# Kernel tuning notes

Measured on AMD Instinct MI355X. Metric: run time of the kernel, lower is better.

## Reference

```python
import jax, jax.numpy as jnp
import numpy as np

CS = 5           # context_size
PAD = CS // 2    # spatial padding
EPS = 1e-12      # torch F.normalize eps


def setup_inputs() -> dict:
    key = jax.random.key(0)
    k1, k2, k3 = jax.random.split(key, 3)
    B, C, H, W = 8, 1024, 64, 64
    OC, INC = 1024, C + CS * CS  # 1049 input channels to 1x1 conv
    feature = jax.random.normal(k1, (B, C, H, W), dtype=jnp.float32)
    conv_w = jax.random.normal(k2, (OC, INC), dtype=jnp.float32) * 0.02
    conv_b = jax.random.normal(k3, (OC,), dtype=jnp.float32) * 0.02
    return {"feature": feature, "conv_w": conv_w, "conv_b": conv_b}


def reference(feature, conv_w, conv_b):
    b, c, h, w = feature.shape
    # L2-normalize over channel dim (torch normalize: x / max(||x||, eps))
    norm = jnp.sqrt(jnp.sum(feature * feature, axis=1, keepdims=True))
    fn = feature / jnp.maximum(norm, EPS)
    fp = jnp.pad(fn, ((0, 0), (0, 0), (PAD, PAD), (PAD, PAD)))
    # Windowed cosine-similarity cost volume: 25 fixed shifts (small static loop)
    sims = []
    for cc in range(CS):      # column shift (outer, matches torch ordering)
        for r in range(CS):   # row shift
            sims.append(jnp.sum(fp[:, :, r:h + r, cc:w + cc] * fn, axis=1))
    vol = jnp.stack(sims, axis=1)              # [b, 25, h, w]
    x = jnp.concatenate([feature, vol], axis=1)  # [b, c+25, h, w]
    # 1x1 conv == per-pixel GEMM over channels
    out = jnp.einsum('bihw,oi->bohw', x, conv_w) + conv_b[None, :, None, None]
    return jax.nn.relu(out)
```

## Files before the change

kernel.cpp:

```cpp
#include <hip/hip_runtime.h>
#include <stdint.h>

#define C_DIM 1024
#define HW    4096
#define KPAD  1056
#define KIN   1049
#define NPIX  32768
#define NCHUNK 16

typedef __bf16 bf16x8 __attribute__((ext_vector_type(8)));
typedef float  f32x4  __attribute__((ext_vector_type(4)));
typedef float  f32x2  __attribute__((ext_vector_type(2)));
typedef unsigned short u16x8 __attribute__((ext_vector_type(8)));

typedef const __attribute__((address_space(1))) void* gas_t;
typedef __attribute__((address_space(3))) void* las_t;

__device__ __forceinline__ unsigned short f2bf(float f) {
  unsigned u = __float_as_uint(f);
  unsigned r = u + 0x7FFFu + ((u >> 16) & 1u);
  return (unsigned short)(r >> 16);
}

__global__ __launch_bounds__(256) void prep_w(const float* __restrict__ cw,
                                              unsigned short* __restrict__ wb) {
  int o = blockIdx.x;
  for (int k = threadIdx.x; k < KPAD; k += 256) {
    float v = (k < KIN) ? cw[(size_t)o * KIN + k] : 0.0f;
    wb[(size_t)o * KPAD + k] = f2bf(v);
  }
}

__global__ __launch_bounds__(256) void pack_norm(const float* __restrict__ feat,
                                                 unsigned short* __restrict__ xb,
                                                 float* __restrict__ inv_norm,
                                                 int p_base) {
  __shared__ float tile[64][65];
  __shared__ float red[4][64];
  int t   = threadIdx.x;
  int p0l = blockIdx.x * 64;
  int p0g = p_base + p0l;
  int b   = p0g >> 12;
  int hw0 = p0g & 4095;
  int pl = t & 63;
  int q  = t >> 6;
  const float* fb = feat + (size_t)b * C_DIM * HW + hw0;
  float sumsq = 0.0f;
  for (int cc = 0; cc < 16; ++cc) {
#pragma unroll
    for (int i = 0; i < 16; ++i) {
      int cl = q + 4 * i;
      float v = fb[(size_t)(cc * 64 + cl) * HW + pl];
      sumsq += v * v;
      tile[cl][pl] = v;
    }
    __syncthreads();
#pragma unroll
    for (int r = 0; r < 2; ++r) {
      int id = t + r * 256;
      int pr = id >> 3;
      int c8 = id & 7;
      u16x8 hv;
#pragma unroll
      for (int e = 0; e < 8; ++e) hv[e] = f2bf(tile[c8 * 8 + e][pr]);
      size_t row = (size_t)(p0l + pr) * KPAD + cc * 64 + c8 * 8;
      *reinterpret_cast<u16x8*>(xb + row) = hv;
    }
    __syncthreads();
  }
  red[q][pl] = sumsq;
  __syncthreads();
  if (t < 64) {
    float s = red[0][t] + red[1][t] + red[2][t] + red[3][t];
    inv_norm[p0g + t] = 1.0f / fmaxf(sqrtf(s), 1e-12f);
  }
}

__global__ __launch_bounds__(256) void corr_part(const float* __restrict__ feat,
                                                 float* __restrict__ part) {
  __shared__ float lds4[4 + 1280 + 4];
  float* tile = lds4 + 4;
  int t = threadIdx.x;
  int bid = blockIdx.x;
  int chunk = bid & 15;
  int strip = (bid >> 4) & 3;
  int b     = bid >> 6;
  int h0 = strip * 16;
  int hr = t >> 4;
  int w0 = (t & 15) * 4;
  int wid = t >> 6;
  int lane = t & 63;

  const float* fb = feat + (size_t)b * C_DIM * HW;
  int rA = t >> 4;
  int cA = (t & 15) * 4;
  int hA = min(max(h0 - 2 + rA, 0), 63);
  int rB = 16 + wid;
  int cB = lane;
  int hB = min(max(h0 - 2 + rB, 0), 63);
  const float* srcA = fb + hA * 64 + cA;
  const float* srcB = fb + hB * 64 + cB;
  float* dstA = tile + wid * 256;
  float* dstB = tile + 1024 + wid * 64;

  float acc[4][25];
#pragma unroll
  for (int j = 0; j < 4; ++j)
#pragma unroll
    for (int k = 0; k < 25; ++k) acc[j][k] = 0.0f;

  int c0 = chunk * 64;
  for (int ci = 0; ci < 64; ++ci) {
    size_t coff = (size_t)(c0 + ci) * HW;
    __builtin_amdgcn_global_load_lds((gas_t)(srcA + coff), (las_t)dstA, 16, 0, 0);
    __builtin_amdgcn_global_load_lds((gas_t)(srcB + coff), (las_t)dstB, 4, 0, 0);
    __syncthreads();

    const float* rp2 = tile + (hr + 2) * 64 + w0;
    f32x4 ctr4 = *reinterpret_cast<const f32x4*>(rp2);
#pragma unroll
    for (int r5 = 0; r5 < 5; ++r5) {
      const float* rp = tile + (hr + r5) * 64 + w0;
      f32x2 eL = *reinterpret_cast<const f32x2*>(rp - 2);
      f32x4 cc4 = *reinterpret_cast<const f32x4*>(rp);
      f32x2 eR = *reinterpret_cast<const f32x2*>(rp + 4);
      float win[8] = {eL[0], eL[1], cc4[0], cc4[1], cc4[2], cc4[3], eR[0], eR[1]};
#pragma unroll
      for (int j = 0; j < 4; ++j)
#pragma unroll
        for (int dcv = 0; dcv < 5; ++dcv)
          acc[j][dcv * 5 + r5] += win[j + dcv] * ctr4[j];
    }
    __syncthreads();
  }

  int p0 = b * 4096 + (h0 + hr) * 64 + w0;
#pragma unroll
  for (int jj = 0; jj < 25; ++jj) {
    f32x4 v = {acc[0][jj], acc[1][jj], acc[2][jj], acc[3][jj]};
    *reinterpret_cast<f32x4*>(&part[(size_t)(chunk * 25 + jj) * NPIX + p0]) = v;
  }
}

__global__ __launch_bounds__(256) void corr_reduce(const float* __restrict__ part,
                                                   const float* __restrict__ inv_norm,
                                                   unsigned short* __restrict__ xb) {
  int pl = blockIdx.x * 256 + threadIdx.x;
  int w = pl & 63, h = (pl >> 6) & 63, b = pl >> 12;
  float inv_c = inv_norm[pl];
  float vals[32];
#pragma unroll
  for (int j = 0; j < 32; ++j) {
    float v = 0.0f;
    if (j < 25) {
      int dc = j / 5 - 2, dr = j % 5 - 2;
      int hh = h + dr, ww = w + dc;
      if (hh >= 0 && hh < 64 && ww >= 0 && ww < 64) {
        float s = 0.0f;
#pragma unroll
        for (int c = 0; c < NCHUNK; ++c)
          s += part[(size_t)(c * 25 + j) * NPIX + pl];
        v = s * inv_c * inv_norm[(b << 12) + (hh << 6) + ww];
      }
    }
    vals[j] = v;
  }
  unsigned short* xp = xb + (size_t)pl * KPAD + 1024;
#pragma unroll
  for (int g = 0; g < 4; ++g) {
    u16x8 pk;
#pragma unroll
    for (int e = 0; e < 8; ++e) pk[e] = f2bf(vals[g * 8 + e]);
    *reinterpret_cast<u16x8*>(xp + g * 8) = pk;
  }
}

__device__ __forceinline__ void stage_tile(const unsigned short* __restrict__ g,
                                           unsigned short* s, int t) {
#pragma unroll
  for (int r = 0; r < 2; ++r) {
    int idx = t + r * 256;
    int row = idx >> 2;
    int q = (idx & 3) ^ ((row >> 1) & 3);
    const unsigned short* gp = g + (size_t)row * KPAD + q * 8;
    unsigned short* sp = s + (t >> 6) * 512 + r * 2048;
    __builtin_amdgcn_global_load_lds((gas_t)gp, (las_t)sp, 16, 0, 0);
  }
}

__global__ __launch_bounds__(256, 2) void gemm_kernel(
    const unsigned short* __restrict__ xb, const unsigned short* __restrict__ wb,
    const float* __restrict__ bias, float* __restrict__ out,
    int p_base, int np) {
  __shared__ __align__(16) unsigned short sA[4096];
  __shared__ __align__(16) unsigned short sB[4096];
  int t = threadIdx.x;
  int lane = t & 63;
  int wid = t >> 6;
  int wm = wid >> 1, wn = wid & 1;
  int l15 = lane & 15, l4 = lane >> 4;
  int bid = blockIdx.x;
  int xcd = bid & 7;
  int j = bid >> 3;
  int o0 = (j & 7) * 128;
  int panel = xcd * (np >> 3) + (j >> 3);
  int p0l = panel * 128;

  f32x4 acc[4][4];
#pragma unroll
  for (int m = 0; m < 4; ++m)
#pragma unroll
    for (int n = 0; n < 4; ++n)
#pragma unroll
      for (int i = 0; i < 4; ++i) acc[m][n][i] = 0.0f;

  const unsigned short* A = wb + (size_t)o0 * KPAD;
  const unsigned short* B = xb + (size_t)p0l * KPAD;

  for (int kt = 0; kt < KPAD / 32; ++kt) {
    int k0 = kt * 32;
    stage_tile(A + k0, sA, t);
    stage_tile(B + k0, sB, t);
    __syncthreads();

    bf16x8 bf[4];
#pragma unroll
    for (int n = 0; n < 4; ++n) {
      int rr = wn * 64 + n * 16 + l15;
      int off = rr * 32 + ((l4 ^ ((rr >> 1) & 3)) * 8);
      bf[n] = *reinterpret_cast<const bf16x8*>(&sB[off]);
    }
#pragma unroll
    for (int m = 0; m < 4; ++m) {
      int ra = wm * 64 + m * 16 + l15;
      int off = ra * 32 + ((l4 ^ ((ra >> 1) & 3)) * 8);
      bf16x8 af = *reinterpret_cast<const bf16x8*>(&sA[off]);
#pragma unroll
      for (int n = 0; n < 4; ++n)
        acc[m][n] = __builtin_amdgcn_mfma_f32_16x16x32_bf16(af, bf[n], acc[m][n], 0, 0, 0);
    }
    __syncthreads();
  }

#pragma unroll
  for (int m = 0; m < 4; ++m) {
    int ob = o0 + wm * 64 + m * 16 + l4 * 4;
    float b0 = bias[ob], b1 = bias[ob + 1], b2 = bias[ob + 2], b3 = bias[ob + 3];
#pragma unroll
    for (int n = 0; n < 4; ++n) {
      int pg = p_base + p0l + wn * 64 + n * 16 + l15;
      int bb = pg >> 12, hw = pg & 4095;
      float* op = out + ((size_t)bb << 22) + hw;
      op[(size_t)(ob + 0) << 12] = fmaxf(acc[m][n][0] + b0, 0.0f);
      op[(size_t)(ob + 1) << 12] = fmaxf(acc[m][n][1] + b1, 0.0f);
      op[(size_t)(ob + 2) << 12] = fmaxf(acc[m][n][2] + b2, 0.0f);
      op[(size_t)(ob + 3) << 12] = fmaxf(acc[m][n][3] + b3, 0.0f);
    }
  }
}

extern "C" void kernel_launch(void* const* d_in, const int* in_sizes, int n_in,
                              void* d_out, int out_size, void* d_ws, size_t ws_size,
                              hipStream_t stream) {
  const float* feat = (const float*)d_in[0];
  const float* cw   = (const float*)d_in[1];
  const float* cb   = (const float*)d_in[2];
  float* out = (float*)d_out;

  char* ws = (char*)d_ws;
  size_t SZ_X = (size_t)NPIX * KPAD * 2;
  size_t SZ_W = (size_t)1024 * KPAD * 2;
  unsigned short* xb = (unsigned short*)(ws);
  unsigned short* wb = (unsigned short*)(ws + SZ_X);
  float* inv_norm    = (float*)(ws + SZ_X + SZ_W);
  float* part        = (float*)(ws + SZ_X + SZ_W + (size_t)NPIX * 4);

  prep_w<<<1024, 256, 0, stream>>>(cw, wb);
  pack_norm<<<512, 256, 0, stream>>>(feat, xb, inv_norm, 0);
  corr_part<<<512, 256, 0, stream>>>(feat, part);
  corr_reduce<<<128, 256, 0, stream>>>(part, inv_norm, xb);
  gemm_kernel<<<2048, 256, 0, stream>>>(xb, wb, cb, out, 0, 256);
}
```

Measured before the change: 429.5 us.

## Double-buffer LDS staging in correlation and GEMM kernels

Both the correlation partial kernel and the bf16 MFMA GEMM now use two LDS buffers. The next channel pair or K-tile is issued with global_load_lds while the current buffer is computed, with a single barrier per step. This is meant to hide global-to-LDS latency and halve barrier stalls. It doubles LDS use per block, which could reduce occupancy, and correctness relies on the barrier waiting for the outstanding async LDS loads.

```diff
diff --git a/kernel.cpp b/kernel.cpp
--- a/kernel.cpp
+++ b/kernel.cpp
@@ -78,8 +78,7 @@
 
 __global__ __launch_bounds__(256) void corr_part(const float* __restrict__ feat,
                                                  float* __restrict__ part) {
-  __shared__ float lds4[4 + 1280 + 4];
-  float* tile = lds4 + 4;
+  __shared__ float lbuf[2][2][1288];
   int t = threadIdx.x;
   int bid = blockIdx.x;
   int chunk = bid & 15;
@@ -100,8 +99,7 @@
   int hB = min(max(h0 - 2 + rB, 0), 63);
   const float* srcA = fb + hA * 64 + cA;
   const float* srcB = fb + hB * 64 + cB;
-  float* dstA = tile + wid * 256;
-  float* dstB = tile + 1024 + wid * 64;
+  int c0 = chunk * 64;
 
   float acc[4][25];
 #pragma unroll
@@ -109,29 +107,46 @@
 #pragma unroll
     for (int k = 0; k < 25; ++k) acc[j][k] = 0.0f;
 
-  int c0 = chunk * 64;
-  for (int ci = 0; ci < 64; ++ci) {
-    size_t coff = (size_t)(c0 + ci) * HW;
-    __builtin_amdgcn_global_load_lds((gas_t)(srcA + coff), (las_t)dstA, 16, 0, 0);
-    __builtin_amdgcn_global_load_lds((gas_t)(srcB + coff), (las_t)dstB, 4, 0, 0);
+  auto stage = [&](int bsel, int csel, int c) {
+    float* dst = &lbuf[bsel][csel][4];
+    size_t coff = (size_t)(c0 + c) * HW;
+    __builtin_amdgcn_global_load_lds((gas_t)(srcA + coff),
+                                     (las_t)(dst + wid * 256), 16, 0, 0);
+    __builtin_amdgcn_global_load_lds((gas_t)(srcB + coff),
+                                     (las_t)(dst + 1024 + wid * 64), 4, 0, 0);
+  };
+
+  stage(0, 0, 0);
+  stage(0, 1, 1);
+  __syncthreads();
+
+  int cur = 0;
+  for (int it = 0; it < 32; ++it) {
+    if (it < 31) {
+      stage(cur ^ 1, 0, 2 * it + 2);
+      stage(cur ^ 1, 1, 2 * it + 3);
+    }
+#pragma unroll
+    for (int cc = 0; cc < 2; ++cc) {
+      const float* tile = &lbuf[cur][cc][4];
+      const float* rp2 = tile + (hr + 2) * 64 + w0;
+      f32x4 ctr4 = *reinterpret_cast<const f32x4*>(rp2);
+#pragma unroll
+      for (int r5 = 0; r5 < 5; ++r5) {
+        const float* rp = tile + (hr + r5) * 64 + w0;
+        f32x2 eL = *reinterpret_cast<const f32x2*>(rp - 2);
+        f32x4 cc4 = *reinterpret_cast<const f32x4*>(rp);
+        f32x2 eR = *reinterpret_cast<const f32x2*>(rp + 4);
+        float win[8] = {eL[0], eL[1], cc4[0], cc4[1], cc4[2], cc4[3], eR[0], eR[1]};
+#pragma unroll
+        for (int j = 0; j < 4; ++j)
+#pragma unroll
+          for (int dcv = 0; dcv < 5; ++dcv)
+            acc[j][dcv * 5 + r5] += win[j + dcv] * ctr4[j];
+      }
+    }
     __syncthreads();
-
-    const float* rp2 = tile + (hr + 2) * 64 + w0;
-    f32x4 ctr4 = *reinterpret_cast<const f32x4*>(rp2);
-#pragma unroll
-    for (int r5 = 0; r5 < 5; ++r5) {
-      const float* rp = tile + (hr + r5) * 64 + w0;
-      f32x2 eL = *reinterpret_cast<const f32x2*>(rp - 2);
-      f32x4 cc4 = *reinterpret_cast<const f32x4*>(rp);
-      f32x2 eR = *reinterpret_cast<const f32x2*>(rp + 4);
-      float win[8] = {eL[0], eL[1], cc4[0], cc4[1], cc4[2], cc4[3], eR[0], eR[1]};
-#pragma unroll
-      for (int j = 0; j < 4; ++j)
-#pragma unroll
-        for (int dcv = 0; dcv < 5; ++dcv)
-          acc[j][dcv * 5 + r5] += win[j + dcv] * ctr4[j];
-    }
-    __syncthreads();
+    cur ^= 1;
   }
 
   int p0 = b * 4096 + (h0 + hr) * 64 + w0;
@@ -192,8 +207,8 @@
     const unsigned short* __restrict__ xb, const unsigned short* __restrict__ wb,
     const float* __restrict__ bias, float* __restrict__ out,
     int p_base, int np) {
-  __shared__ __align__(16) unsigned short sA[4096];
-  __shared__ __align__(16) unsigned short sB[4096];
+  __shared__ __align__(16) unsigned short sA[2][4096];
+  __shared__ __align__(16) unsigned short sB[2][4096];
   int t = threadIdx.x;
   int lane = t & 63;
   int wid = t >> 6;
@@ -217,29 +232,35 @@
   const unsigned short* A = wb + (size_t)o0 * KPAD;
   const unsigned short* B = xb + (size_t)p0l * KPAD;
 
-  for (int kt = 0; kt < KPAD / 32; ++kt) {
-    int k0 = kt * 32;
-    stage_tile(A + k0, sA, t);
-    stage_tile(B + k0, sB, t);
-    __syncthreads();
-
+  stage_tile(A, sA[0], t);
+  stage_tile(B, sB[0], t);
+  __syncthreads();
+
+  int cur = 0;
+  const int NKT = KPAD / 32;
+  for (int kt = 0; kt < NKT; ++kt) {
+    if (kt + 1 < NKT) {
+      stage_tile(A + (kt + 1) * 32, sA[cur ^ 1], t);
+      stage_tile(B + (kt + 1) * 32, sB[cur ^ 1], t);
+    }
     bf16x8 bf[4];
 #pragma unroll
     for (int n = 0; n < 4; ++n) {
       int rr = wn * 64 + n * 16 + l15;
       int off = rr * 32 + ((l4 ^ ((rr >> 1) & 3)) * 8);
-      bf[n] = *reinterpret_cast<const bf16x8*>(&sB[off]);
+      bf[n] = *reinterpret_cast<const bf16x8*>(&sB[cur][off]);
     }
 #pragma unroll
     for (int m = 0; m < 4; ++m) {
       int ra = wm * 64 + m * 16 + l15;
       int off = ra * 32 + ((l4 ^ ((ra >> 1) & 3)) * 8);
-      bf16x8 af = *reinterpret_cast<const bf16x8*>(&sA[off]);
+      bf16x8 af = *reinterpret_cast<const bf16x8*>(&sA[cur][off]);
 #pragma unroll
       for (int n = 0; n < 4; ++n)
         acc[m][n] = __builtin_amdgcn_mfma_f32_16x16x32_bf16(af, bf[n], acc[m][n], 0, 0, 0);
     }
     __syncthreads();
+    cur ^= 1;
   }
 
 #pragma unroll
```

Measured after the change: 412.8 us. 1.04x faster.
